# Performance work log

Hardware: AMD Instinct MI355X
Metric: run time of the kernel (lower is better)

## Reference

```python
import jax, jax.numpy as jnp
import numpy as np


def setup_inputs() -> dict:
    key = jax.random.key(0)
    k1, k2, k3 = jax.random.split(key, 3)
    B, Cin, Cout, L, K = 16, 64, 64, 65536, 3
    return {
        "x": jax.random.normal(k1, (B, Cin, L), dtype=jnp.float32),
        "alpha": jnp.zeros((1, Cin, 1), dtype=jnp.float32),
        "weight": jax.random.normal(k2, (Cout, Cin, K), dtype=jnp.float32),
        "weight_scale": jnp.ones((Cout, 1, 1), dtype=jnp.float32),
        "bias": jax.random.normal(k3, (Cout,), dtype=jnp.float32),
        "beta": jnp.ones((1, Cout, 1), dtype=jnp.float32),
        "gamma": jnp.zeros((1, Cout, 1), dtype=jnp.float32),
        "zeta": jnp.zeros((1, Cout, 1), dtype=jnp.float32),
    }


def _rsign(x, alpha):
    # forward: sign(x - alpha) in {-1,+1}; backward: identity w.r.t. x (STE)
    signed = jnp.where(x >= alpha, 1.0, -1.0).astype(x.dtype)
    return x + jax.lax.stop_gradient(signed - x)


def _clipped_ste_sign(w):
    # forward: sign(w); backward: grad passes only where |w| <= 1 (Bi-RealNet)
    w_bin = jnp.sign(w)
    mask = (jnp.abs(w) <= 1.0).astype(w.dtype)
    wm = w * mask
    return jax.lax.stop_gradient(w_bin) + wm - jax.lax.stop_gradient(wm)


def _rprelu(x, beta, gamma, zeta):
    xs = x - gamma
    return jnp.where(x > gamma, xs + zeta, beta * xs + zeta)


def reference(x, alpha, weight, weight_scale, bias, beta, gamma, zeta):
    # RSign -> scaled binary conv1d (stride=1, pad=1) -> RPReLU
    xb = _rsign(x, alpha)                        # [B,Cin,L], values +-1
    wb = _clipped_ste_sign(weight) * weight_scale  # [Cout,Cin,K]
    y = jax.lax.conv_general_dilated(
        xb, wb, window_strides=(1,), padding=[(1, 1)],
        dimension_numbers=("NCH", "OIH", "NCH"))  # [B,Cout,L]
    y = y + bias[None, :, None]
    return _rprelu(y, beta, gamma, zeta)
```

## Files before the change

### kernel.cpp

```cpp
#include <hip/hip_runtime.h>

#define LLEN 65536
#define CIN 64
#define COUT 64
#define BROW (LLEN + 8)
#define NBLK_A (LLEN / 2048)

typedef float f32x4 __attribute__((ext_vector_type(4)));
typedef unsigned long long u64;
typedef u64 u64x4 __attribute__((ext_vector_type(4)));

struct __align__(64) WRec {
    u64 p0, p1, p2;
    float A;
    float S;
    float Bv, G, Z;
    float f0, f2;
    float pad[3];
};

__device__ __forceinline__ void pack_weights_body(
        const float* __restrict__ w, const float* __restrict__ wscale,
        const float* __restrict__ bias, const float* __restrict__ beta,
        const float* __restrict__ gamma, const float* __restrict__ zeta,
        WRec* __restrict__ rec) {
    int co = threadIdx.x;
    if (co >= COUT) return;
    const float* wr = w + co * (CIN * 3);
    u64 p[3] = {0, 0, 0}, nzw[3] = {0, 0, 0};
    #pragma unroll
    for (int q = 0; q < 4; ++q) {
        f32x4 buf[12];
        #pragma unroll
        for (int j = 0; j < 12; ++j)
            buf[j] = *(const f32x4*)(wr + q * 48 + 4 * j);
        #pragma unroll
        for (int j = 0; j < 12; ++j) {
            #pragma unroll
            for (int m = 0; m < 4; ++m) {
                const int idx = q * 48 + 4 * j + m;
                const int ci = idx / 3, k = idx % 3;
                const float wv = buf[j][m];
                p[k]   |= ((u64)(wv > 0.0f)) << ci;
                nzw[k] |= ((u64)(wv != 0.0f)) << ci;
            }
        }
    }
    const int n0 = __popcll(nzw[0]), n1 = __popcll(nzw[1]), n2 = __popcll(nzw[2]);
    WRec r;
    float s = wscale[co];
    r.p0 = p[0]; r.p1 = p[1]; r.p2 = p[2];
    r.A  = s * (float)(n0 + n1 + n2) + bias[co];
    r.S  = -2.0f * s;
    r.Bv = beta[co]; r.G = gamma[co]; r.Z = zeta[co];
    r.f0 = 0.5f * (float)n0;
    r.f2 = 0.5f * (float)n2;
    r.pad[0] = r.pad[1] = r.pad[2] = 0.0f;
    rec[co] = r;
}

__global__ void __launch_bounds__(256) pack_x(
        const float* __restrict__ x,
        const float* __restrict__ alpha,
        u64* __restrict__ bits,
        const float* __restrict__ w,
        const float* __restrict__ wscale,
        const float* __restrict__ bias,
        const float* __restrict__ beta,
        const float* __restrict__ gamma,
        const float* __restrict__ zeta,
        WRec* __restrict__ rec) {
    if (blockIdx.x == NBLK_A) {
        if (blockIdx.y == 0)
            pack_weights_body(w, wscale, bias, beta, gamma, zeta, rec);
        return;
    }
    const int t = threadIdx.x;
    const int b = blockIdx.y;
    const int l0 = blockIdx.x * 2048;
    const float* xb = x + (size_t)b * CIN * LLEN + l0 + 4 * t;

    u64 wa0 = 0, wa1 = 0, wa2 = 0, wa3 = 0;
    u64 wb0 = 0, wb1 = 0, wb2 = 0, wb3 = 0;
    #pragma unroll
    for (int q = 0; q < 16; ++q) {
        f32x4 blo[4], bhi[4];
        #pragma unroll
        for (int j = 0; j < 4; ++j) {
            const float* rp = xb + (size_t)(q * 4 + j) * LLEN;
            blo[j] = __builtin_nontemporal_load((const f32x4*)rp);
            bhi[j] = __builtin_nontemporal_load((const f32x4*)(rp + 1024));
        }
        #pragma unroll
        for (int j = 0; j < 4; ++j) {
            const int ci = q * 4 + j;
            const float a = alpha[ci];
            wa0 |= ((u64)(blo[j].x >= a)) << ci;
            wa1 |= ((u64)(blo[j].y >= a)) << ci;
            wa2 |= ((u64)(blo[j].z >= a)) << ci;
            wa3 |= ((u64)(blo[j].w >= a)) << ci;
            wb0 |= ((u64)(bhi[j].x >= a)) << ci;
            wb1 |= ((u64)(bhi[j].y >= a)) << ci;
            wb2 |= ((u64)(bhi[j].z >= a)) << ci;
            wb3 |= ((u64)(bhi[j].w >= a)) << ci;
        }
    }
    u64* dst = bits + (size_t)b * BROW + l0 + 4 * t + 4;
    u64x4 va; va.x = wa0; va.y = wa1; va.z = wa2; va.w = wa3;
    u64x4 vb; vb.x = wb0; vb.y = wb1; vb.z = wb2; vb.w = wb3;
    *(u64x4*)dst = va;
    *(u64x4*)(dst + 1024) = vb;
}

__device__ __forceinline__ float rprelu(float y, float B, float G, float Z) {
    float xs = y - G;
    return (y > G) ? (xs + Z) : fmaf(B, xs, Z);
}

__global__ void __launch_bounds__(256) bconv_compute(
        const u64* __restrict__ bits,
        const WRec* __restrict__ rec,
        float* __restrict__ out) {
    const int t     = threadIdx.x;
    const int chunk = blockIdx.x;
    const int co    = blockIdx.y;
    const int b     = blockIdx.z;
    const int c0    = chunk * 8192;

    const WRec r = rec[co];
    const u64* base = bits + (size_t)b * BROW + c0 + 4 * t;
    float* outp = out + ((size_t)b * COUT + co) * LLEN + c0 + 4 * t;

    const bool lo = (chunk == 0) && (t == 0);
    const bool hi = (chunk == 7) && (t == 255);

    #pragma unroll 4
    for (int j = 0; j < 8; ++j) {
        const u64* src = base + 1024 * j;
        const u64 xq0 = src[3], xq1 = src[4], xq2 = src[5],
                  xq3 = src[6], xq4 = src[7], xq5 = src[8];

        float fx = (float)(__popcll(xq0 ^ r.p0) + __popcll(xq1 ^ r.p1)
                         + __popcll(xq2 ^ r.p2));
        float fy = (float)(__popcll(xq1 ^ r.p0) + __popcll(xq2 ^ r.p1)
                         + __popcll(xq3 ^ r.p2));
        float fz = (float)(__popcll(xq2 ^ r.p0) + __popcll(xq3 ^ r.p1)
                         + __popcll(xq4 ^ r.p2));
        float fw = (float)(__popcll(xq3 ^ r.p0) + __popcll(xq4 ^ r.p1)
                         + __popcll(xq5 ^ r.p2));
        if (j == 0 && lo)
            fx = (float)(__popcll(xq1 ^ r.p1) + __popcll(xq2 ^ r.p2)) + r.f0;
        if (j == 7 && hi)
            fw = (float)(__popcll(xq3 ^ r.p0) + __popcll(xq4 ^ r.p1)) + r.f2;

        f32x4 o;
        o.x = rprelu(fmaf(r.S, fx, r.A), r.Bv, r.G, r.Z);
        o.y = rprelu(fmaf(r.S, fy, r.A), r.Bv, r.G, r.Z);
        o.z = rprelu(fmaf(r.S, fz, r.A), r.Bv, r.G, r.Z);
        o.w = rprelu(fmaf(r.S, fw, r.A), r.Bv, r.G, r.Z);
        __builtin_nontemporal_store(o, (f32x4*)(outp + 1024 * j));
    }
}

extern "C" void kernel_launch(void* const* d_in, const int* in_sizes, int n_in,
                              void* d_out, int out_size, void* d_ws, size_t ws_size,
                              hipStream_t stream) {
    const float* x      = (const float*)d_in[0];
    const float* alpha  = (const float*)d_in[1];
    const float* w      = (const float*)d_in[2];
    const float* wscale = (const float*)d_in[3];
    const float* bias   = (const float*)d_in[4];
    const float* beta   = (const float*)d_in[5];
    const float* gamma  = (const float*)d_in[6];
    const float* zeta   = (const float*)d_in[7];
    float* out = (float*)d_out;

    WRec* rec = (WRec*)d_ws;
    u64* bits = (u64*)((char*)d_ws + 4096);

    dim3 gridA(NBLK_A + 1, 16);
    pack_x<<<gridA, 256, 0, stream>>>(x, alpha, bits, w, wscale, bias,
                                      beta, gamma, zeta, rec);

    dim3 gridB(8, COUT, 16);
    bconv_compute<<<gridB, 256, 0, stream>>>(bits, rec, out);
}
```

Baseline: 102.7 us.

## Pack input as per-channel bitplanes via ballot and transpose in LDS

The pack kernel now gives each block one input channel and uses wavefront ballots to write per-channel bitplanes, so reads stay contiguous along L. The conv kernel loads a tile of bitplanes, transposes 64x64 bit blocks with shuffle-xor butterfly steps, and stores the channel-packed words in padded shared memory. Each thread then loops over all 64 output channels, reusing the loaded packed input instead of having separate blocks per output channel re-read it. The cost is extra shuffle and transpose work and a grid with far fewer blocks in the second kernel.

```diff
diff --git a/kernel.cpp b/kernel.cpp
--- a/kernel.cpp
+++ b/kernel.cpp
@@ -3,12 +3,12 @@
 #define LLEN 65536
 #define CIN 64
 #define COUT 64
-#define BROW (LLEN + 8)
-#define NBLK_A (LLEN / 2048)
+#define BPW 1024
+#define CHUNK 2048
+#define NTILE (CHUNK / 64 + 2)
 
 typedef float f32x4 __attribute__((ext_vector_type(4)));
 typedef unsigned long long u64;
-typedef u64 u64x4 __attribute__((ext_vector_type(4)));
 
 struct __align__(64) WRec {
     u64 p0, p1, p2;
@@ -59,57 +59,36 @@
     rec[co] = r;
 }
 
-__global__ void __launch_bounds__(256) pack_x(
-        const float* __restrict__ x,
-        const float* __restrict__ alpha,
-        u64* __restrict__ bits,
-        const float* __restrict__ w,
-        const float* __restrict__ wscale,
-        const float* __restrict__ bias,
-        const float* __restrict__ beta,
-        const float* __restrict__ gamma,
-        const float* __restrict__ zeta,
+__global__ void __launch_bounds__(256) pack_bitplane(
+        const float* __restrict__ x, const float* __restrict__ alpha,
+        u64* __restrict__ bp,
+        const float* __restrict__ w, const float* __restrict__ wscale,
+        const float* __restrict__ bias, const float* __restrict__ beta,
+        const float* __restrict__ gamma, const float* __restrict__ zeta,
         WRec* __restrict__ rec) {
-    if (blockIdx.x == NBLK_A) {
+    if (blockIdx.x == CIN) {
         if (blockIdx.y == 0)
             pack_weights_body(w, wscale, bias, beta, gamma, zeta, rec);
         return;
     }
-    const int t = threadIdx.x;
-    const int b = blockIdx.y;
-    const int l0 = blockIdx.x * 2048;
-    const float* xb = x + (size_t)b * CIN * LLEN + l0 + 4 * t;
+    const int lane = threadIdx.x & 63;
+    const int wv   = threadIdx.x >> 6;
+    const int ci = blockIdx.x, b = blockIdx.y;
+    const float a = alpha[ci];
+    const float* xr = x + ((size_t)b * CIN + ci) * LLEN + wv * 16384;
+    u64* bpr = bp + ((size_t)b * CIN + ci) * BPW + wv * 256;
 
-    u64 wa0 = 0, wa1 = 0, wa2 = 0, wa3 = 0;
-    u64 wb0 = 0, wb1 = 0, wb2 = 0, wb3 = 0;
     #pragma unroll
-    for (int q = 0; q < 16; ++q) {
-        f32x4 blo[4], bhi[4];
+    for (int g = 0; g < 4; ++g) {
+        u64 acc = 0;
         #pragma unroll
-        for (int j = 0; j < 4; ++j) {
-            const float* rp = xb + (size_t)(q * 4 + j) * LLEN;
-            blo[j] = __builtin_nontemporal_load((const f32x4*)rp);
-            bhi[j] = __builtin_nontemporal_load((const f32x4*)(rp + 1024));
+        for (int s = 0; s < 64; ++s) {
+            float v = __builtin_nontemporal_load(xr + g * 4096 + s * 64 + lane);
+            u64 bal = __ballot(v >= a);
+            if (lane == s) acc = bal;
         }
-        #pragma unroll
-        for (int j = 0; j < 4; ++j) {
-            const int ci = q * 4 + j;
-            const float a = alpha[ci];
-            wa0 |= ((u64)(blo[j].x >= a)) << ci;
-            wa1 |= ((u64)(blo[j].y >= a)) << ci;
-            wa2 |= ((u64)(blo[j].z >= a)) << ci;
-            wa3 |= ((u64)(blo[j].w >= a)) << ci;
-            wb0 |= ((u64)(bhi[j].x >= a)) << ci;
-            wb1 |= ((u64)(bhi[j].y >= a)) << ci;
-            wb2 |= ((u64)(bhi[j].z >= a)) << ci;
-            wb3 |= ((u64)(bhi[j].w >= a)) << ci;
-        }
+        bpr[g * 64 + lane] = acc;
     }
-    u64* dst = bits + (size_t)b * BROW + l0 + 4 * t + 4;
-    u64x4 va; va.x = wa0; va.y = wa1; va.z = wa2; va.w = wa3;
-    u64x4 vb; vb.x = wb0; vb.y = wb1; vb.z = wb2; vb.w = wb3;
-    *(u64x4*)dst = va;
-    *(u64x4*)(dst + 1024) = vb;
 }
 
 __device__ __forceinline__ float rprelu(float y, float B, float G, float Z) {
@@ -117,48 +96,69 @@
     return (y > G) ? (xs + Z) : fmaf(B, xs, Z);
 }
 
-__global__ void __launch_bounds__(256) bconv_compute(
-        const u64* __restrict__ bits,
-        const WRec* __restrict__ rec,
+__device__ __forceinline__ u64 xstep(u64 v, u64 y, int lane, int d, u64 m) {
+    return ((lane & d) == 0) ? ((v & m) | ((y & m) << d))
+                             : ((v & ~m) | ((y >> d) & m));
+}
+
+__global__ void __launch_bounds__(512) bconv2(
+        const u64* __restrict__ bp, const WRec* __restrict__ rec,
         float* __restrict__ out) {
-    const int t     = threadIdx.x;
-    const int chunk = blockIdx.x;
-    const int co    = blockIdx.y;
-    const int b     = blockIdx.z;
-    const int c0    = chunk * 8192;
+    __shared__ u64 wlds[NTILE * 64 + ((NTILE * 64) >> 2) + 2];
+    const int t = threadIdx.x;
+    const int lane = t & 63, wv = t >> 6;
+    const int chunk = blockIdx.x, b = blockIdx.y;
+    const int c0 = chunk * CHUNK;
+    const int W0 = c0 / 64 - 1;
 
-    const WRec r = rec[co];
-    const u64* base = bits + (size_t)b * BROW + c0 + 4 * t;
-    float* outp = out + ((size_t)b * COUT + co) * LLEN + c0 + 4 * t;
+    for (int T = wv; T < NTILE; T += 8) {
+        const int W = W0 + T;
+        u64 v = 0;
+        if (W >= 0 && W < BPW)
+            v = bp[((size_t)b * CIN + lane) * BPW + W];
+        u64 y;
+        y = (u64)__shfl_xor((long long)v, 32); v = xstep(v, y, lane, 32, 0x00000000FFFFFFFFull);
+        y = (u64)__shfl_xor((long long)v, 16); v = xstep(v, y, lane, 16, 0x0000FFFF0000FFFFull);
+        y = (u64)__shfl_xor((long long)v,  8); v = xstep(v, y, lane,  8, 0x00FF00FF00FF00FFull);
+        y = (u64)__shfl_xor((long long)v,  4); v = xstep(v, y, lane,  4, 0x0F0F0F0F0F0F0F0Full);
+        y = (u64)__shfl_xor((long long)v,  2); v = xstep(v, y, lane,  2, 0x3333333333333333ull);
+        y = (u64)__shfl_xor((long long)v,  1); v = xstep(v, y, lane,  1, 0x5555555555555555ull);
+        const int lp = T * 64 + lane;
+        wlds[lp + (lp >> 2)] = v;
+    }
+    __syncthreads();
 
+    u64 xq[6];
+    #pragma unroll
+    for (int k = 0; k < 6; ++k) {
+        const int lp = 4 * t + 63 + k;
+        xq[k] = wlds[lp + (lp >> 2)];
+    }
     const bool lo = (chunk == 0) && (t == 0);
-    const bool hi = (chunk == 7) && (t == 255);
+    const bool hi = (chunk == gridDim.x - 1) && (t == 511);
+    float* outp = out + (size_t)b * COUT * LLEN + c0 + 4 * t;
 
     #pragma unroll 4
-    for (int j = 0; j < 8; ++j) {
-        const u64* src = base + 1024 * j;
-        const u64 xq0 = src[3], xq1 = src[4], xq2 = src[5],
-                  xq3 = src[6], xq4 = src[7], xq5 = src[8];
-
-        float fx = (float)(__popcll(xq0 ^ r.p0) + __popcll(xq1 ^ r.p1)
-                         + __popcll(xq2 ^ r.p2));
-        float fy = (float)(__popcll(xq1 ^ r.p0) + __popcll(xq2 ^ r.p1)
-                         + __popcll(xq3 ^ r.p2));
-        float fz = (float)(__popcll(xq2 ^ r.p0) + __popcll(xq3 ^ r.p1)
-                         + __popcll(xq4 ^ r.p2));
-        float fw = (float)(__popcll(xq3 ^ r.p0) + __popcll(xq4 ^ r.p1)
-                         + __popcll(xq5 ^ r.p2));
-        if (j == 0 && lo)
-            fx = (float)(__popcll(xq1 ^ r.p1) + __popcll(xq2 ^ r.p2)) + r.f0;
-        if (j == 7 && hi)
-            fw = (float)(__popcll(xq3 ^ r.p0) + __popcll(xq4 ^ r.p1)) + r.f2;
-
+    for (int co = 0; co < COUT; ++co) {
+        const WRec r = rec[co];
+        float fx = (float)(__popcll(xq[0] ^ r.p0) + __popcll(xq[1] ^ r.p1)
+                         + __popcll(xq[2] ^ r.p2));
+        float fy = (float)(__popcll(xq[1] ^ r.p0) + __popcll(xq[2] ^ r.p1)
+                         + __popcll(xq[3] ^ r.p2));
+        float fz = (float)(__popcll(xq[2] ^ r.p0) + __popcll(xq[3] ^ r.p1)
+                         + __popcll(xq[4] ^ r.p2));
+        float fw = (float)(__popcll(xq[3] ^ r.p0) + __popcll(xq[4] ^ r.p1)
+                         + __popcll(xq[5] ^ r.p2));
+        if (lo)
+            fx = (float)(__popcll(xq[1] ^ r.p1) + __popcll(xq[2] ^ r.p2)) + r.f0;
+        if (hi)
+            fw = (float)(__popcll(xq[3] ^ r.p0) + __popcll(xq[4] ^ r.p1)) + r.f2;
         f32x4 o;
         o.x = rprelu(fmaf(r.S, fx, r.A), r.Bv, r.G, r.Z);
         o.y = rprelu(fmaf(r.S, fy, r.A), r.Bv, r.G, r.Z);
         o.z = rprelu(fmaf(r.S, fz, r.A), r.Bv, r.G, r.Z);
         o.w = rprelu(fmaf(r.S, fw, r.A), r.Bv, r.G, r.Z);
-        __builtin_nontemporal_store(o, (f32x4*)(outp + 1024 * j));
+        __builtin_nontemporal_store(o, (f32x4*)(outp + (size_t)co * LLEN));
     }
 }
 
@@ -176,12 +176,12 @@
     float* out = (float*)d_out;
 
     WRec* rec = (WRec*)d_ws;
-    u64* bits = (u64*)((char*)d_ws + 4096);
+    u64* bp = (u64*)((char*)d_ws + 4096);
 
-    dim3 gridA(NBLK_A + 1, 16);
-    pack_x<<<gridA, 256, 0, stream>>>(x, alpha, bits, w, wscale, bias,
-                                      beta, gamma, zeta, rec);
+    dim3 gridA(CIN + 1, 16);
+    pack_bitplane<<<gridA, 256, 0, stream>>>(x, alpha, bp, w, wscale, bias,
+                                             beta, gamma, zeta, rec);
 
-    dim3 gridB(8, COUT, 16);
-    bconv_compute<<<gridB, 256, 0, stream>>>(bits, rec, out);
+    dim3 gridB(LLEN / CHUNK, 16);
+    bconv2<<<gridB, 512, 0, stream>>>(bp, rec, out);
 }
```

Result: slower. 203.6 us (+98.2%).
